# Kernel tuning notes

Hardware: AMD Instinct MI355X
Metric: run time of the kernel (lower is better)

Reference implementation:

```python
import jax, jax.numpy as jnp
import numpy as np

POS_DIM = 60  # position_embed_dim


def sincos_pos_embed(pos, dim):
    # pos: [..., 3] -> [..., dim]; dim//3 channels per coordinate, half sin / half cos
    d = dim // 3            # 20
    half = d // 2           # 10
    omega = 1.0 / (10000.0 ** (jnp.arange(half, dtype=pos.dtype) / half))
    out = pos[..., None] * omega                     # [..., 3, half]
    emb = jnp.concatenate([jnp.sin(out), jnp.cos(out)], axis=-1)  # [..., 3, d]
    return emb.reshape(pos.shape[:-1] + (3 * d,))


def setup_inputs() -> dict:
    key = jax.random.key(0)
    ks = jax.random.split(key, 20)
    B, N, K = 2, 16384, 24
    d_points, d_model = 64, 128
    s = 0.02
    inp = {
        "features": jax.random.normal(ks[0], (B, N, d_points), jnp.float32),
        "xyz": jax.random.normal(ks[1], (B, N, 3), jnp.float32),
        "knn_idx": jax.random.randint(ks[2], (B, N, K), 0, N),
        "knn_xyz": jax.random.normal(ks[3], (B, N, K, 3), jnp.float32),
        "fc1_w": jax.random.normal(ks[4], (d_points, d_model), jnp.float32) * s,
        "fc1_b": jnp.zeros((d_model,), jnp.float32),
        "fc2_w": jax.random.normal(ks[5], (d_model, d_model), jnp.float32) * s,
        "fc2_b": jnp.zeros((d_model,), jnp.float32),
        "d1_w": jax.random.normal(ks[6], (POS_DIM, d_model), jnp.float32) * s,
        "d1_b": jnp.zeros((d_model,), jnp.float32),
        "d2_w": jax.random.normal(ks[7], (d_model, d_model), jnp.float32) * s,
        "d2_b": jnp.zeros((d_model,), jnp.float32),
        "g1_w": jax.random.normal(ks[8], (d_model, d_model), jnp.float32) * s,
        "g1_b": jnp.zeros((d_model,), jnp.float32),
        "g2_w": jax.random.normal(ks[9], (d_model, d_model), jnp.float32) * s,
        "g2_b": jnp.zeros((d_model,), jnp.float32),
    }
    return inp


def reference(features, xyz, knn_idx, knn_xyz,
              fc1_w, fc1_b, fc2_w, fc2_b,
              d1_w, d1_b, d2_w, d2_b,
              g1_w, g1_b, g2_w, g2_b):
    B = features.shape[0]
    x = features @ fc1_w + fc1_b                       # [B,N,D]
    # index_points: gather neighbor features (q=x, k=v=gathered)
    kv = x[jnp.arange(B)[:, None, None], knn_idx]      # [B,N,K,D]
    g_xyz = xyz[:, :, None] - knn_xyz                  # [B,N,K,3]
    g_emb = sincos_pos_embed(g_xyz, POS_DIM)           # [B,N,K,60]
    pos_enc = jax.nn.relu(g_emb @ d1_w + d1_b) @ d2_w + d2_b   # [B,N,K,D]
    h = x[:, :, None] - kv + pos_enc                   # [B,N,K,D]
    attn = jax.nn.relu(h @ g1_w + g1_b) @ g2_w + g2_b  # [B,N,K,D]
    attn = jax.nn.softmax(attn / np.sqrt(kv.shape[-1]), axis=-2)  # softmax over K
    res = jnp.einsum('bmnf,bmnf->bmf', attn, kv + pos_enc)
    res = res @ fc2_w + fc2_b + x
    return res, attn
```

## Files before the change

kernel.cpp:

```cpp
#include <hip/hip_runtime.h>
#include <hip/hip_bf16.h>
#include <math.h>

constexpr int BB = 2;
constexpr int NN = 16384;
constexpr int KK = 24;
constexpr int DM = 128;
constexpr int DP = 64;

constexpr int PPB = 4;
constexpr int RR  = PPB * KK;

typedef __bf16 v8bf __attribute__((ext_vector_type(8)));
typedef float  v4f  __attribute__((ext_vector_type(4)));

constexpr int LDA128 = 136;
constexpr int LDA64  = 72;

constexpr int OFF_FC1T = 0;
constexpr int OFF_D1T  = 8192;
constexpr int OFF_D2T  = 16384;
constexpr int OFF_G1T  = 32768;
constexpr int OFF_G2T  = 49152;
constexpr int OFF_FC2T = 65536;
constexpr int W_TOTAL  = 81920;

__global__ __launch_bounds__(256) void prep_kernel(
    const float* __restrict__ fc1_w, const float* __restrict__ fc2_w,
    const float* __restrict__ d1_w,  const float* __restrict__ d2_w,
    const float* __restrict__ g1_w,  const float* __restrict__ g2_w,
    __hip_bfloat16* __restrict__ wbuf)
{
    const int i = blockIdx.x * 256 + threadIdx.x;
    if (i >= W_TOTAL) return;
    float v;
    if (i < OFF_D1T) {
        const int j = i, n = j >> 6, k = j & 63;
        v = fc1_w[k * DM + n];
    } else if (i < OFF_D2T) {
        const int j = i - OFF_D1T, n = j >> 6, k = j & 63;
        v = (k < 60) ? d1_w[k * DM + n] : 0.f;
    } else if (i < OFF_G1T) {
        const int j = i - OFF_D2T, n = j >> 7, k = j & 127;
        v = d2_w[k * DM + n];
    } else if (i < OFF_G2T) {
        const int j = i - OFF_G1T, n = j >> 7, k = j & 127;
        v = g1_w[k * DM + n];
    } else if (i < OFF_FC2T) {
        const int j = i - OFF_G2T, n = j >> 7, k = j & 127;
        v = g2_w[k * DM + n];
    } else {
        const int j = i - OFF_FC2T, f = j >> 7, g = j & 127;
        v = fc2_w[g * DM + f];
    }
    wbuf[i] = __float2bfloat16(v);
}

template <int MT, int NKT, int LDA, int LDB>
__device__ __forceinline__ void mm_frags(
    const __hip_bfloat16* As, const __hip_bfloat16* __restrict__ Bt,
    int c0, int lane, v4f (&acc)[MT][2])
{
    const int ln = lane & 15, quad = lane >> 4;
    #pragma unroll
    for (int mt = 0; mt < MT; ++mt) {
        acc[mt][0] = (v4f)0.f;
        acc[mt][1] = (v4f)0.f;
    }
    #pragma unroll
    for (int kt = 0; kt < NKT; ++kt) {
        const int k0 = kt * 32 + quad * 8;
        const v8bf b0 = *(const v8bf*)(Bt + (c0 + ln) * LDB + k0);
        const v8bf b1 = *(const v8bf*)(Bt + (c0 + 16 + ln) * LDB + k0);
        #pragma unroll
        for (int mt = 0; mt < MT; ++mt) {
            const v8bf a = *(const v8bf*)(As + (mt * 16 + ln) * LDA + k0);
            acc[mt][0] = __builtin_amdgcn_mfma_f32_16x16x32_bf16(a, b0, acc[mt][0], 0, 0, 0);
            acc[mt][1] = __builtin_amdgcn_mfma_f32_16x16x32_bf16(a, b1, acc[mt][1], 0, 0, 0);
        }
    }
}

__global__ __launch_bounds__(256) void fc1_kernel(
    const float* __restrict__ feat,
    const __hip_bfloat16* __restrict__ fc1t,
    const float* __restrict__ fc1_b,
    __hip_bfloat16* __restrict__ x_bf)
{
    __shared__ alignas(16) __hip_bfloat16 s_f[32 * LDA64];
    const int tid = threadIdx.x;
    const int r0  = blockIdx.x * 32;
    for (int e = tid; e < 32 * DP; e += 256) {
        const int r = e >> 6, k = e & 63;
        s_f[r * LDA64 + k] = __float2bfloat16(feat[(size_t)(r0 + r) * DP + k]);
    }
    __syncthreads();
    const int w = tid >> 6, lane = tid & 63;
    const int ln = lane & 15, quad = lane >> 4;
    const int c0 = w * 32;
    v4f acc[2][2];
    mm_frags<2, 2, LDA64, 64>(s_f, fc1t, c0, lane, acc);
    #pragma unroll
    for (int nl = 0; nl < 2; ++nl) {
        const int col = c0 + nl * 16 + ln;
        const float bb = fc1_b[col];
        #pragma unroll
        for (int mt = 0; mt < 2; ++mt)
            #pragma unroll
            for (int r = 0; r < 4; ++r) {
                const int row = mt * 16 + quad * 4 + r;
                x_bf[(size_t)(r0 + row) * DM + col] = __float2bfloat16(acc[mt][nl][r] + bb);
            }
    }
}

__device__ __forceinline__ int zoff(int row, int col) {
    return (row << 7) + ((((col >> 3) ^ row) & 15) << 3) + (col & 7);
}

__global__ __launch_bounds__(256) void fused_kernel(
    const __hip_bfloat16* __restrict__ x_bf,
    const float* __restrict__ xyz,
    const int*   __restrict__ knn_idx,
    const float* __restrict__ knn_xyz,
    const __hip_bfloat16* __restrict__ wbuf,
    const float* __restrict__ d1_b, const float* __restrict__ d2_b,
    const float* __restrict__ g1_b, const float* __restrict__ g2_b,
    const float* __restrict__ fc2_b,
    float* __restrict__ out_res,
    float* __restrict__ out_attn)
{
    __shared__ alignas(16) __hip_bfloat16 s_X[RR * LDA128];
    __shared__ alignas(16) __hip_bfloat16 s_Y[RR * LDA128];
    __shared__ alignas(16) __hip_bfloat16 s_Z[RR * DM];
    __shared__ float s_xm[PPB * DM];

    __hip_bfloat16* s_ge = s_X;
    int*   s_idx = reinterpret_cast<int*>(s_X + RR * LDA64);
    float* s_res = reinterpret_cast<float*>(s_Y);

    const int tid = threadIdx.x;
    const int pt0 = blockIdx.x * PPB;
    const int b   = pt0 >> 14;
    const int w = tid >> 6, lane = tid & 63;
    const int ln = lane & 15, quad = lane >> 4;
    const int c0 = w * 32;

    if (tid < RR) s_idx[tid] = knn_idx[(size_t)pt0 * KK + tid];
    if (tid < PPB * DM / 8) {
        const v8bf xv = *(const v8bf*)(x_bf + (size_t)pt0 * DM + tid * 8);
        #pragma unroll
        for (int j = 0; j < 8; ++j) s_xm[tid * 8 + j] = (float)xv[j];
    }
    if (tid < RR)
        *reinterpret_cast<uint2*>(s_ge + tid * LDA64 + 60) = make_uint2(0u, 0u);
    for (int e = tid; e < RR * 30; e += 256) {
        const int row = e / 30;
        const int rem = e - row * 30;
        const int c = rem / 10;
        const int i = rem - c * 10;
        const int g = pt0 + row / 24;
        const float pv = xyz[(size_t)g * 3 + c] - knn_xyz[((size_t)pt0 * KK + row) * 3 + c];
        const float om = exp2f(-(float)i * 1.3287712379549449f);
        float sv, cv;
        __sincosf(pv * om, &sv, &cv);
        s_ge[row * LDA64 + c * 20 + i]      = __float2bfloat16(sv);
        s_ge[row * LDA64 + c * 20 + 10 + i] = __float2bfloat16(cv);
    }
    __syncthreads();

    v4f acc[6][2];

    v8bf gv[6];
    {
        const size_t xbase = (size_t)b * NN * DM;
        #pragma unroll
        for (int i = 0; i < 6; ++i) {
            const int e = tid + i * 256;
            const int row = e >> 4, part = e & 15;
            gv[i] = *(const v8bf*)(x_bf + xbase + (size_t)s_idx[row] * DM + part * 8);
        }
    }
    mm_frags<6, 2, LDA64, 64>(s_ge, wbuf + OFF_D1T, c0, lane, acc);
    #pragma unroll
    for (int i = 0; i < 6; ++i) {
        const int e = tid + i * 256;
        const int row = e >> 4, part = e & 15;
        *reinterpret_cast<v8bf*>(&s_Z[zoff(row, part * 8)]) = gv[i];
    }
    {
        const float bb0 = d1_b[c0 + ln], bb1 = d1_b[c0 + 16 + ln];
        #pragma unroll
        for (int mt = 0; mt < 6; ++mt) {
            const int row0 = mt * 16 + quad * 4;
            #pragma unroll
            for (int r = 0; r < 4; ++r) {
                s_Y[(row0 + r) * LDA128 + c0 + ln]      = __float2bfloat16(fmaxf(acc[mt][0][r] + bb0, 0.f));
                s_Y[(row0 + r) * LDA128 + c0 + 16 + ln] = __float2bfloat16(fmaxf(acc[mt][1][r] + bb1, 0.f));
            }
        }
    }
    __syncthreads();

    mm_frags<6, 4, LDA128, DM>(s_Y, wbuf + OFF_D2T, c0, lane, acc);
    {
        const float bb0 = d2_b[c0 + ln], bb1 = d2_b[c0 + 16 + ln];
        #pragma unroll
        for (int mt = 0; mt < 6; ++mt) {
            const int row0 = mt * 16 + quad * 4;
            const int p = row0 / 24;
            const float xm0 = s_xm[p * DM + c0 + ln];
            const float xm1 = s_xm[p * DM + c0 + 16 + ln];
            #pragma unroll
            for (int r = 0; r < 4; ++r) {
                const int row = row0 + r;
                const int zo0 = zoff(row, c0 + ln);
                const int zo1 = zoff(row, c0 + 16 + ln);
                const float pe0 = acc[mt][0][r] + bb0;
                const float pe1 = acc[mt][1][r] + bb1;
                const float kv0 = __bfloat162float(s_Z[zo0]);
                const float kv1 = __bfloat162float(s_Z[zo1]);
                s_X[row * LDA128 + c0 + ln]      = __float2bfloat16(xm0 - kv0 + pe0);
                s_X[row * LDA128 + c0 + 16 + ln] = __float2bfloat16(xm1 - kv1 + pe1);
                s_Z[zo0] = __float2bfloat16(kv0 + pe0);
                s_Z[zo1] = __float2bfloat16(kv1 + pe1);
            }
        }
    }
    __syncthreads();

    mm_frags<6, 4, LDA128, DM>(s_X, wbuf + OFF_G1T, c0, lane, acc);
    {
        const float bb0 = g1_b[c0 + ln], bb1 = g1_b[c0 + 16 + ln];
        #pragma unroll
        for (int mt = 0; mt < 6; ++mt) {
            const int row0 = mt * 16 + quad * 4;
            #pragma unroll
            for (int r = 0; r < 4; ++r) {
                s_Y[(row0 + r) * LDA128 + c0 + ln]      = __float2bfloat16(fmaxf(acc[mt][0][r] + bb0, 0.f));
                s_Y[(row0 + r) * LDA128 + c0 + 16 + ln] = __float2bfloat16(fmaxf(acc[mt][1][r] + bb1, 0.f));
            }
        }
    }
    __syncthreads();

    mm_frags<6, 4, LDA128, DM>(s_Y, wbuf + OFF_G2T, c0, lane, acc);
    {
        const float iscl = 0.08838834764831845f;
        const float bb0 = g2_b[c0 + ln], bb1 = g2_b[c0 + 16 + ln];
        #pragma unroll
        for (int mt = 0; mt < 6; ++mt) {
            const int row0 = mt * 16 + quad * 4;
            #pragma unroll
            for (int r = 0; r < 4; ++r) {
                s_X[(row0 + r) * LDA128 + c0 + ln]      = __float2bfloat16((acc[mt][0][r] + bb0) * iscl);
                s_X[(row0 + r) * LDA128 + c0 + 16 + ln] = __float2bfloat16((acc[mt][1][r] + bb1) * iscl);
            }
        }
    }
    __syncthreads();

    #pragma unroll
    for (int cc = 0; cc < 2; ++cc) {
        const int ch = cc * 256 + tid;
        const int p = ch >> 7, f = ch & 127;
        const int rbase = p * KK;
        float lv[KK];
        float mx = -1e30f;
        #pragma unroll
        for (int n = 0; n < KK; ++n) {
            lv[n] = __bfloat162float(s_X[(rbase + n) * LDA128 + f]);
            mx = fmaxf(mx, lv[n]);
        }
        float sum = 0.f;
        #pragma unroll
        for (int n = 0; n < KK; ++n) {
            const float ev = __expf(lv[n] - mx);
            lv[n] = ev;
            sum += ev;
        }
        const float inv = 1.f / sum;
        float racc = 0.f;
        float* ab = out_attn + (size_t)(pt0 + p) * KK * DM + f;
        #pragma unroll
        for (int n = 0; n < KK; ++n) {
            const float a = lv[n] * inv;
            ab[n * DM] = a;
            racc = fmaf(a, __bfloat162float(s_Z[zoff(rbase + n, f)]), racc);
        }
        s_res[ch] = racc;
    }
    __syncthreads();

    #pragma unroll
    for (int cc = 0; cc < 2; ++cc) {
        const int ch = cc * 256 + tid;
        const int p = ch >> 7, f = ch & 127;
        const v8bf* wr = reinterpret_cast<const v8bf*>(wbuf + OFF_FC2T + f * DM);
        float a2 = 0.f;
        #pragma unroll
        for (int g8 = 0; g8 < 16; ++g8) {
            const v8bf wv = wr[g8];
            const v4f r0 = *(const v4f*)(s_res + p * DM + g8 * 8);
            const v4f r1 = *(const v4f*)(s_res + p * DM + g8 * 8 + 4);
            #pragma unroll
            for (int j = 0; j < 4; ++j) {
                a2 = fmaf(r0[j], (float)wv[j], a2);
                a2 = fmaf(r1[j], (float)wv[j + 4], a2);
            }
        }
        out_res[(size_t)(pt0 + p) * DM + f] = a2 + fc2_b[f] + s_xm[p * DM + f];
    }
}

extern "C" void kernel_launch(void* const* d_in, const int* in_sizes, int n_in,
                              void* d_out, int out_size, void* d_ws, size_t ws_size,
                              hipStream_t stream)
{
    const float* features = (const float*)d_in[0];
    const float* xyz      = (const float*)d_in[1];
    const int*   knn_idx  = (const int*)  d_in[2];
    const float* knn_xyz  = (const float*)d_in[3];
    const float* fc1_w    = (const float*)d_in[4];
    const float* fc1_b    = (const float*)d_in[5];
    const float* fc2_w    = (const float*)d_in[6];
    const float* fc2_b    = (const float*)d_in[7];
    const float* d1_w     = (const float*)d_in[8];
    const float* d1_b     = (const float*)d_in[9];
    const float* d2_w     = (const float*)d_in[10];
    const float* d2_b     = (const float*)d_in[11];
    const float* g1_w     = (const float*)d_in[12];
    const float* g1_b     = (const float*)d_in[13];
    const float* g2_w     = (const float*)d_in[14];
    const float* g2_b     = (const float*)d_in[15];

    __hip_bfloat16* x_bf = (__hip_bfloat16*)d_ws;
    __hip_bfloat16* wbuf = x_bf + (size_t)BB * NN * DM;
    float* out_res  = (float*)d_out;
    float* out_attn = out_res + (size_t)BB * NN * DM;

    prep_kernel<<<(W_TOTAL + 255) / 256, 256, 0, stream>>>(
        fc1_w, fc2_w, d1_w, d2_w, g1_w, g2_w, wbuf);
    fc1_kernel<<<(BB * NN) / 32, 256, 0, stream>>>(
        features, wbuf + OFF_FC1T, fc1_b, x_bf);
    fused_kernel<<<(BB * NN) / PPB, 256, 0, stream>>>(
        x_bf, xyz, knn_idx, knn_xyz, wbuf,
        d1_b, d2_b, g1_b, g2_b, fc2_b, out_res, out_attn);
}
```

Before: 804.2 us.

## Merge LDS staging buffers to raise occupancy and use MFMA for fc2

Collapses the two activation staging buffers into one shared buffer and stores the per-point x rows as bf16, cutting LDS per block so three blocks can fit per CU (launch_bounds 256,3). Extra barriers are added so each buffer is not overwritten while another wave still reads it. The final fc2 projection now runs as a padded MFMA on bf16 residuals instead of a scalar FMA loop. MFMA loops are also wrapped with s_setprio. Risks are more barriers, possible register spills under the tighter bound, and lower precision from rounding residuals to bf16.

```diff
diff --git a/kernel.cpp b/kernel.cpp
--- a/kernel.cpp
+++ b/kernel.cpp
@@ -67,6 +67,7 @@
         acc[mt][0] = (v4f)0.f;
         acc[mt][1] = (v4f)0.f;
     }
+    __builtin_amdgcn_s_setprio(1);
     #pragma unroll
     for (int kt = 0; kt < NKT; ++kt) {
         const int k0 = kt * 32 + quad * 8;
@@ -79,6 +80,7 @@
             acc[mt][1] = __builtin_amdgcn_mfma_f32_16x16x32_bf16(a, b1, acc[mt][1], 0, 0, 0);
         }
     }
+    __builtin_amdgcn_s_setprio(0);
 }
 
 __global__ __launch_bounds__(256) void fc1_kernel(
@@ -118,7 +120,7 @@
     return (row << 7) + ((((col >> 3) ^ row) & 15) << 3) + (col & 7);
 }
 
-__global__ __launch_bounds__(256) void fused_kernel(
+__global__ __launch_bounds__(256, 3) void fused_kernel(
     const __hip_bfloat16* __restrict__ x_bf,
     const float* __restrict__ xyz,
     const int*   __restrict__ knn_idx,
@@ -130,14 +132,12 @@
     float* __restrict__ out_res,
     float* __restrict__ out_attn)
 {
-    __shared__ alignas(16) __hip_bfloat16 s_X[RR * LDA128];
-    __shared__ alignas(16) __hip_bfloat16 s_Y[RR * LDA128];
+    __shared__ alignas(16) __hip_bfloat16 s_A[RR * LDA128];
     __shared__ alignas(16) __hip_bfloat16 s_Z[RR * DM];
-    __shared__ float s_xm[PPB * DM];
-
-    __hip_bfloat16* s_ge = s_X;
-    int*   s_idx = reinterpret_cast<int*>(s_X + RR * LDA64);
-    float* s_res = reinterpret_cast<float*>(s_Y);
+    __shared__ alignas(16) __hip_bfloat16 s_xm[PPB * DM];
+
+    __hip_bfloat16* s_ge = s_A;
+    int* s_idx = reinterpret_cast<int*>(s_A + RR * LDA64);
 
     const int tid = threadIdx.x;
     const int pt0 = blockIdx.x * PPB;
@@ -147,11 +147,9 @@
     const int c0 = w * 32;
 
     if (tid < RR) s_idx[tid] = knn_idx[(size_t)pt0 * KK + tid];
-    if (tid < PPB * DM / 8) {
-        const v8bf xv = *(const v8bf*)(x_bf + (size_t)pt0 * DM + tid * 8);
-        #pragma unroll
-        for (int j = 0; j < 8; ++j) s_xm[tid * 8 + j] = (float)xv[j];
-    }
+    if (tid < PPB * DM / 8)
+        *reinterpret_cast<v8bf*>(s_xm + tid * 8) =
+            *(const v8bf*)(x_bf + (size_t)pt0 * DM + tid * 8);
     if (tid < RR)
         *reinterpret_cast<uint2*>(s_ge + tid * LDA64 + 60) = make_uint2(0u, 0u);
     for (int e = tid; e < RR * 30; e += 256) {
@@ -181,13 +179,14 @@
             gv[i] = *(const v8bf*)(x_bf + xbase + (size_t)s_idx[row] * DM + part * 8);
         }
     }
-    mm_frags<6, 2, LDA64, 64>(s_ge, wbuf + OFF_D1T, c0, lane, acc);
+    mm_frags<6, 2, LDA64, 64>(s_A, wbuf + OFF_D1T, c0, lane, acc);
     #pragma unroll
     for (int i = 0; i < 6; ++i) {
         const int e = tid + i * 256;
         const int row = e >> 4, part = e & 15;
         *reinterpret_cast<v8bf*>(&s_Z[zoff(row, part * 8)]) = gv[i];
     }
+    __syncthreads();
     {
         const float bb0 = d1_b[c0 + ln], bb1 = d1_b[c0 + 16 + ln];
         #pragma unroll
@@ -195,22 +194,23 @@
             const int row0 = mt * 16 + quad * 4;
             #pragma unroll
             for (int r = 0; r < 4; ++r) {
-                s_Y[(row0 + r) * LDA128 + c0 + ln]      = __float2bfloat16(fmaxf(acc[mt][0][r] + bb0, 0.f));
-                s_Y[(row0 + r) * LDA128 + c0 + 16 + ln] = __float2bfloat16(fmaxf(acc[mt][1][r] + bb1, 0.f));
-            }
-        }
-    }
-    __syncthreads();
-
-    mm_frags<6, 4, LDA128, DM>(s_Y, wbuf + OFF_D2T, c0, lane, acc);
+                s_A[(row0 + r) * LDA128 + c0 + ln]      = __float2bfloat16(fmaxf(acc[mt][0][r] + bb0, 0.f));
+                s_A[(row0 + r) * LDA128 + c0 + 16 + ln] = __float2bfloat16(fmaxf(acc[mt][1][r] + bb1, 0.f));
+            }
+        }
+    }
+    __syncthreads();
+
+    mm_frags<6, 4, LDA128, DM>(s_A, wbuf + OFF_D2T, c0, lane, acc);
+    __syncthreads();
     {
         const float bb0 = d2_b[c0 + ln], bb1 = d2_b[c0 + 16 + ln];
         #pragma unroll
         for (int mt = 0; mt < 6; ++mt) {
             const int row0 = mt * 16 + quad * 4;
             const int p = row0 / 24;
-            const float xm0 = s_xm[p * DM + c0 + ln];
-            const float xm1 = s_xm[p * DM + c0 + 16 + ln];
+            const float xm0 = __bfloat162float(s_xm[p * DM + c0 + ln]);
+            const float xm1 = __bfloat162float(s_xm[p * DM + c0 + 16 + ln]);
             #pragma unroll
             for (int r = 0; r < 4; ++r) {
                 const int row = row0 + r;
@@ -220,8 +220,8 @@
                 const float pe1 = acc[mt][1][r] + bb1;
                 const float kv0 = __bfloat162float(s_Z[zo0]);
                 const float kv1 = __bfloat162float(s_Z[zo1]);
-                s_X[row * LDA128 + c0 + ln]      = __float2bfloat16(xm0 - kv0 + pe0);
-                s_X[row * LDA128 + c0 + 16 + ln] = __float2bfloat16(xm1 - kv1 + pe1);
+                s_A[row * LDA128 + c0 + ln]      = __float2bfloat16(xm0 - kv0 + pe0);
+                s_A[row * LDA128 + c0 + 16 + ln] = __float2bfloat16(xm1 - kv1 + pe1);
                 s_Z[zo0] = __float2bfloat16(kv0 + pe0);
                 s_Z[zo1] = __float2bfloat16(kv1 + pe1);
             }
@@ -229,7 +229,8 @@
     }
     __syncthreads();
 
-    mm_frags<6, 4, LDA128, DM>(s_X, wbuf + OFF_G1T, c0, lane, acc);
+    mm_frags<6, 4, LDA128, DM>(s_A, wbuf + OFF_G1T, c0, lane, acc);
+    __syncthreads();
     {
         const float bb0 = g1_b[c0 + ln], bb1 = g1_b[c0 + 16 + ln];
         #pragma unroll
@@ -237,14 +238,15 @@
             const int row0 = mt * 16 + quad * 4;
             #pragma unroll
             for (int r = 0; r < 4; ++r) {
-                s_Y[(row0 + r) * LDA128 + c0 + ln]      = __float2bfloat16(fmaxf(acc[mt][0][r] + bb0, 0.f));
-                s_Y[(row0 + r) * LDA128 + c0 + 16 + ln] = __float2bfloat16(fmaxf(acc[mt][1][r] + bb1, 0.f));
-            }
-        }
-    }
-    __syncthreads();
-
-    mm_frags<6, 4, LDA128, DM>(s_Y, wbuf + OFF_G2T, c0, lane, acc);
+                s_A[(row0 + r) * LDA128 + c0 + ln]      = __float2bfloat16(fmaxf(acc[mt][0][r] + bb0, 0.f));
+                s_A[(row0 + r) * LDA128 + c0 + 16 + ln] = __float2bfloat16(fmaxf(acc[mt][1][r] + bb1, 0.f));
+            }
+        }
+    }
+    __syncthreads();
+
+    mm_frags<6, 4, LDA128, DM>(s_A, wbuf + OFF_G2T, c0, lane, acc);
+    __syncthreads();
     {
         const float iscl = 0.08838834764831845f;
         const float bb0 = g2_b[c0 + ln], bb1 = g2_b[c0 + 16 + ln];
@@ -253,13 +255,14 @@
             const int row0 = mt * 16 + quad * 4;
             #pragma unroll
             for (int r = 0; r < 4; ++r) {
-                s_X[(row0 + r) * LDA128 + c0 + ln]      = __float2bfloat16((acc[mt][0][r] + bb0) * iscl);
-                s_X[(row0 + r) * LDA128 + c0 + 16 + ln] = __float2bfloat16((acc[mt][1][r] + bb1) * iscl);
-            }
-        }
-    }
-    __syncthreads();
-
+                s_A[(row0 + r) * LDA128 + c0 + ln]      = __float2bfloat16((acc[mt][0][r] + bb0) * iscl);
+                s_A[(row0 + r) * LDA128 + c0 + 16 + ln] = __float2bfloat16((acc[mt][1][r] + bb1) * iscl);
+            }
+        }
+    }
+    __syncthreads();
+
+    float rres[2];
     #pragma unroll
     for (int cc = 0; cc < 2; ++cc) {
         const int ch = cc * 256 + tid;
@@ -269,7 +272,7 @@
         float mx = -1e30f;
         #pragma unroll
         for (int n = 0; n < KK; ++n) {
-            lv[n] = __bfloat162float(s_X[(rbase + n) * LDA128 + f]);
+            lv[n] = __bfloat162float(s_A[(rbase + n) * LDA128 + f]);
             mx = fmaxf(mx, lv[n]);
         }
         float sum = 0.f;
@@ -288,28 +291,31 @@
             ab[n * DM] = a;
             racc = fmaf(a, __bfloat162float(s_Z[zoff(rbase + n, f)]), racc);
         }
-        s_res[ch] = racc;
-    }
-    __syncthreads();
-
+        rres[cc] = racc;
+    }
+    __syncthreads();
     #pragma unroll
     for (int cc = 0; cc < 2; ++cc) {
         const int ch = cc * 256 + tid;
         const int p = ch >> 7, f = ch & 127;
-        const v8bf* wr = reinterpret_cast<const v8bf*>(wbuf + OFF_FC2T + f * DM);
-        float a2 = 0.f;
-        #pragma unroll
-        for (int g8 = 0; g8 < 16; ++g8) {
-            const v8bf wv = wr[g8];
-            const v4f r0 = *(const v4f*)(s_res + p * DM + g8 * 8);
-            const v4f r1 = *(const v4f*)(s_res + p * DM + g8 * 8 + 4);
-            #pragma unroll
-            for (int j = 0; j < 4; ++j) {
-                a2 = fmaf(r0[j], (float)wv[j], a2);
-                a2 = fmaf(r1[j], (float)wv[j + 4], a2);
-            }
-        }
-        out_res[(size_t)(pt0 + p) * DM + f] = a2 + fc2_b[f] + s_xm[p * DM + f];
+        s_A[p * LDA128 + f] = __float2bfloat16(rres[cc]);
+    }
+    __syncthreads();
+
+    {
+        v4f a2[1][2];
+        mm_frags<1, 4, LDA128, DM>(s_A, wbuf + OFF_FC2T, c0, lane, a2);
+        if (quad == 0) {
+            #pragma unroll
+            for (int nl = 0; nl < 2; ++nl) {
+                const int col = c0 + nl * 16 + ln;
+                const float bb = fc2_b[col];
+                #pragma unroll
+                for (int r = 0; r < 4; ++r)
+                    out_res[(size_t)(pt0 + r) * DM + col] =
+                        a2[0][nl][r] + bb + __bfloat162float(s_xm[r * DM + col]);
+            }
+        }
     }
 }
 
```

Result: faster. 675.9 us (-16.0%).
